# Kernel optimization log

Measured on AMD Instinct MI355X. Metric: run time of the kernel, lower is better.

## Reference

```python
import jax, jax.numpy as jnp
import numpy as np

THRESH = 0.5
DECAY = 0.2
D_IN = 784
H1 = 2048
H2 = 10
K = 10
U = D_IN + H1
L = 128
B = 1024


def setup_inputs() -> dict:
    key = jax.random.key(0)
    ks = jax.random.split(key, 6)
    inp = jax.random.uniform(ks[0], (B, D_IN), dtype=jnp.float32)
    W1 = jax.random.normal(ks[1], (H1, D_IN), dtype=jnp.float32) * 0.05
    b1 = jnp.zeros((H1,), dtype=jnp.float32)
    W2 = jax.random.normal(ks[2], (H2, H1), dtype=jnp.float32) * 0.05
    b2 = jnp.zeros((H2,), dtype=jnp.float32)
    # core_mem_all[k][u][0] -> sparse-ish per-unit vector, [1] -> count
    core_mem_vec = (jax.random.uniform(ks[3], (K, U, L)) > 0.7).astype(jnp.float32)
    core_mem_cnt = jax.random.randint(ks[4], (K, U), 0, 5).astype(jnp.int32)
    return {"input": inp, "W1": W1, "b1": b1, "W2": W2, "b2": b2,
            "core_mem_vec": core_mem_vec, "core_mem_cnt": core_mem_cnt,
            "time_window": 20}


def act_fun(mem):
    # spike = Heaviside(mem - thresh)
    return (mem > THRESH).astype(mem.dtype)


def reference(input, W1, b1, W2, b2, core_mem_vec, core_mem_cnt, time_window):
    batch, d_in = input.shape
    h1 = W1.shape[0]
    h2 = W2.shape[0]
    Lv = core_mem_vec.shape[-1]

    # Precompute, per (core k, unit u): contribution to count_add_1 / count_add_2
    # when unit u spikes. count_add_1 += (last nonzero index of temp) - 1 when cnt>0;
    # count_add_2 += cnt when cnt>0. Sum over cores up front (loop order irrelevant).
    nz = core_mem_vec != 0                                     # [K,U,L]
    has = nz.any(-1)
    last_idx = Lv - 1 - jnp.argmax(nz[..., ::-1].astype(jnp.int32), axis=-1)  # [K,U]
    active = (core_mem_cnt > 0) & has
    val1 = jnp.where(active, last_idx - 1, 0).sum(0).astype(jnp.float32)      # [U]
    val2 = jnp.where(core_mem_cnt > 0, core_mem_cnt, 0).sum(0).astype(jnp.float32)
    v1x, v1h = val1[:d_in], val1[d_in:]
    v2x, v2h = val2[:d_in], val2[d_in:]

    key = jax.random.key(42)

    def step(carry, t):
        h1m, h1s, h2m, h2s, h2sum, a1, a2, cs = carry
        # Bernoulli rate encoding of the input image
        x = (input > jax.random.uniform(jax.random.fold_in(key, t), input.shape)).astype(jnp.float32)
        # mem_update: mem = mem*decay*(1-spike) + W x + b ; spike = mem > thresh
        h1m = h1m * DECAY * (1.0 - h1s) + x @ W1.T + b1
        h1s = act_fun(h1m)
        h2m = h2m * DECAY * (1.0 - h2s) + h1s @ W2.T + b2
        h2s = act_fun(h2m)
        h2sum = h2sum + h2s
        # vectorized core-memory gather/count: sum per-unit precomputed values
        # over all spiking units, across the batch
        xs = x.sum(0)      # [784] spike counts per input unit this step
        hs = h1s.sum(0)    # [h1]
        a1 = a1 + xs @ v1x + hs @ v1h
        a2 = a2 + xs @ v2x + hs @ v2h
        cs = cs + xs.sum() + hs.sum()
        return (h1m, h1s, h2m, h2s, h2sum, a1, a2, cs), None

    z1 = jnp.zeros((batch, h1), dtype=jnp.float32)
    z2 = jnp.zeros((batch, h2), dtype=jnp.float32)
    carry = (z1, z1, z2, z2, z2, jnp.float32(0), jnp.float32(0), jnp.float32(0))
    carry, _ = jax.lax.scan(step, carry, jnp.arange(time_window))
    _, _, _, _, h2sum, a1, a2, cs = carry
    outputs = h2sum / time_window
    return outputs, a1, a2, cs
```

## Files before the change

### kernel.cpp

```cpp
#include <hip/hip_runtime.h>
#include <cstdint>
#include <cstddef>

static constexpr int D_IN = 784;
static constexpr int H1   = 2048;
static constexpr int H2   = 10;
static constexpr int KK   = 10;
static constexpr int UU   = 2832;
static constexpr int LL   = 128;
static constexpr int BB   = 1024;
static constexpr int TT   = 20;
static constexpr int HALF = BB * D_IN / 2;
static constexpr int NCH  = 25;
static constexpr int NLIMB = 3;
static constexpr int XA_T  = 32 * NCH * 64;
static constexpr int BITS_T = BB * 64;
static constexpr int PANEL = NCH * NLIMB * 64;
static constexpr int NPART_GEN = 2000;
static constexpr int NPART_H1  = 256;
static constexpr int NPART = NPART_GEN + NPART_H1;

static constexpr int BLK_VALS  = UU / 4;
static constexpr int BLK_W2T   = H1 / 256;
static constexpr int BLK_LIMBS = (64 * NCH * 64) / 256;
static constexpr int BLK_TRANS = 16 * 13;
static constexpr int SETUP_BLOCKS = BLK_VALS + BLK_W2T + BLK_LIMBS + BLK_TRANS;

typedef int v4i  __attribute__((ext_vector_type(4)));
typedef int v16i __attribute__((ext_vector_type(16)));

#define MFMA_I8 __builtin_amdgcn_mfma_i32_32x32x32_i8

__device__ __forceinline__ uint32_t rotl32(uint32_t x, int d) {
  return (x << d) | (x >> (32 - d));
}
__device__ __forceinline__ void threefry2x32(uint32_t k0, uint32_t k1,
                                             uint32_t& x0, uint32_t& x1) {
  uint32_t ks2 = k0 ^ k1 ^ 0x1BD11BDAu;
  x0 += k0; x1 += k1;
#define TF_R(r) { x0 += x1; x1 = rotl32(x1, (r)); x1 ^= x0; }
  TF_R(13) TF_R(15) TF_R(26) TF_R(6)
  x0 += k1;  x1 += ks2 + 1u;
  TF_R(17) TF_R(29) TF_R(16) TF_R(24)
  x0 += ks2; x1 += k0 + 2u;
  TF_R(13) TF_R(15) TF_R(26) TF_R(6)
  x0 += k0;  x1 += k1 + 3u;
  TF_R(17) TF_R(29) TF_R(16) TF_R(24)
  x0 += k1;  x1 += ks2 + 4u;
  TF_R(13) TF_R(15) TF_R(26) TF_R(6)
  x0 += ks2; x1 += k0 + 5u;
#undef TF_R
}
__device__ __forceinline__ float bits_to_unif(uint32_t b) {
  uint32_t fb = (b >> 9) | 0x3F800000u;
  return __uint_as_float(fb) - 1.0f;
}

__device__ __forceinline__ double wave_red(double v) {
  #pragma unroll
  for (int off = 32; off > 0; off >>= 1) v += __shfl_down(v, off, 64);
  return v;
}
__device__ __forceinline__ void block_store3(double s0, double s1, double s2,
                                             double* slot) {
  __shared__ double lds[3][8];
  int lane = threadIdx.x & 63, w = threadIdx.x >> 6;
  int nw = (int)(blockDim.x >> 6);
  s0 = wave_red(s0); s1 = wave_red(s1); s2 = wave_red(s2);
  if (lane == 0) { lds[0][w] = s0; lds[1][w] = s1; lds[2][w] = s2; }
  __syncthreads();
  if (threadIdx.x == 0) {
    double t0 = 0, t1 = 0, t2 = 0;
    for (int i = 0; i < nw; i++) { t0 += lds[0][i]; t1 += lds[1][i]; t2 += lds[2][i]; }
    slot[0] = t0; slot[1] = t1; slot[2] = t2;
  }
}

__global__ __launch_bounds__(256)
void setup(const float* __restrict__ cmv, const int* __restrict__ cmc,
           float* __restrict__ v1, float* __restrict__ v2,
           const float* __restrict__ W2, float* __restrict__ W2T,
           const float* __restrict__ W1, v4i* __restrict__ W1L,
           const float* __restrict__ input, float2* __restrict__ inT2) {
  int bx = blockIdx.x;
  if (bx < BLK_VALS) {
    int u = bx * 4 + (threadIdx.x >> 6);
    int lane = threadIdx.x & 63;
    float acc1 = 0.0f, acc2 = 0.0f;
    for (int k = 0; k < KK; k++) {
      const float* p = cmv + ((size_t)k * UU + u) * LL;
      float a = p[lane];
      float b = p[lane + 64];
      unsigned long long mlo = __ballot(a != 0.0f);
      unsigned long long mhi = __ballot(b != 0.0f);
      int c = cmc[k * UU + u];
      if (c > 0) {
        int last = mhi ? (127 - __builtin_clzll(mhi))
                       : (mlo ? (63 - __builtin_clzll(mlo)) : -1);
        if (last >= 0) acc1 += (float)(last - 1);
        acc2 += (float)c;
      }
    }
    if (lane == 0) { v1[u] = acc1; v2[u] = acc2; }
  } else if (bx < BLK_VALS + BLK_W2T) {
    int i = (bx - BLK_VALS) * 256 + threadIdx.x;
    #pragma unroll
    for (int j = 0; j < H2; j++) W2T[i * H2 + j] = W2[j * H1 + i];
  } else if (bx < BLK_VALS + BLK_W2T + BLK_LIMBS) {
    int tid = (bx - BLK_VALS - BLK_W2T) * 256 + threadIdx.x;
    int lane = tid & 63;
    int tc = tid >> 6;
    int n = ((tc / NCH) << 5) + (lane & 31);
    int chunk = tc % NCH;
    int k0 = chunk * 32 + (lane >> 5) * 16;
    union { v4i v; signed char b[16]; } d[NLIMB];
    #pragma unroll
    for (int j = 0; j < 16; j++) {
      long long F = 0;
      int k = k0 + j;
      if (k < D_IN) {
        double w = (double)W1[(size_t)n * D_IN + k];
        F = llround(w * 0x1p24);
        if (F >  8355711LL) F =  8355711LL;
        if (F < -8421504LL) F = -8421504LL;
      }
      #pragma unroll
      for (int l = 0; l < NLIMB; l++) {
        int dig = (int)((F + 128) & 255) - 128;
        d[l].b[j] = (signed char)dig;
        F = (F - dig) >> 8;
      }
    }
    #pragma unroll
    for (int l = 0; l < NLIMB; l++) W1L[(size_t)(tc * NLIMB + l) * 64 + lane] = d[l].v;
  } else {
    int tile = bx - (BLK_VALS + BLK_W2T + BLK_LIMBS);
    int tm = tile / 13, tk = tile % 13;
    int mb = tm * 32, k0 = tk * 64;
    int ncol = (tk == 12) ? 16 : 64;
    __shared__ float ts[64][65];
    int tid = threadIdx.x;
    if (tk == 12) {
      for (int idx = tid; idx < 64 * 4; idx += 256) {
        int r = idx >> 2, c4 = idx & 3;
        int m = mb + (r & 31) + ((r >> 5) << 9);
        const float4* src = (const float4*)(input + (size_t)m * D_IN + k0 + c4 * 4);
        float4 vq = *src;
        ts[r][c4 * 4 + 0] = vq.x; ts[r][c4 * 4 + 1] = vq.y;
        ts[r][c4 * 4 + 2] = vq.z; ts[r][c4 * 4 + 3] = vq.w;
      }
    } else {
      for (int idx = tid; idx < 64 * 16; idx += 256) {
        int r = idx >> 4, c4 = idx & 15;
        int m = mb + (r & 31) + ((r >> 5) << 9);
        const float4* src = (const float4*)(input + (size_t)m * D_IN + k0 + c4 * 4);
        float4 vq = *src;
        ts[r][c4 * 4 + 0] = vq.x; ts[r][c4 * 4 + 1] = vq.y;
        ts[r][c4 * 4 + 2] = vq.z; ts[r][c4 * 4 + 3] = vq.w;
      }
    }
    __syncthreads();
    for (int idx = tid; idx < ncol * 32; idx += 256) {
      int kr = idx >> 5, mc = idx & 31;
      inT2[(size_t)(k0 + kr) * 512 + mb + mc] =
          make_float2(ts[mc][kr], ts[32 + mc][kr]);
    }
  }
}

__global__ __launch_bounds__(256)
void gen_all(const float2* __restrict__ inT2, v4i* __restrict__ XA,
             const float* __restrict__ v1, const float* __restrict__ v2,
             double* __restrict__ gpart) {
  int t  = blockIdx.x / 100;
  int gw = (blockIdx.x % 100) * 4 + (threadIdx.x >> 6);
  int lane = threadIdx.x & 63;
  int mtile = gw / NCH, chunk = gw - mtile * NCH;
  int m = (mtile << 5) + (lane & 31);
  int k0 = chunk * 32 + (lane >> 5) * 16;
  uint32_t f0 = 0u, f1 = (uint32_t)t;
  threefry2x32(0u, 42u, f0, f1);
  union { v4i v; unsigned char b[16]; } r0, r1;
  double s0 = 0, s1 = 0, s2 = 0;
  v4i* XA_t = XA + (size_t)t * XA_T;
  if (k0 < D_IN) {
    #pragma unroll
    for (int j = 0; j < 16; j++) {
      int k = k0 + j;
      uint32_t c0 = (uint32_t)(m * D_IN + k), c1 = c0 + (uint32_t)HALF;
      threefry2x32(f0, f1, c0, c1);
      float u0 = bits_to_unif(c0), u1 = bits_to_unif(c1);
      float2 iv = inT2[(size_t)k * 512 + m];
      unsigned char x0 = (iv.x > u0) ? 1 : 0;
      unsigned char x1 = (iv.y > u1) ? 1 : 0;
      r0.b[j] = x0; r1.b[j] = x1;
      double xsum = (double)(x0 + x1);
      s0 += xsum * (double)v1[k];
      s1 += xsum * (double)v2[k];
      s2 += xsum;
    }
  } else {
    r0.v = (v4i){0, 0, 0, 0};
    r1.v = (v4i){0, 0, 0, 0};
  }
  XA_t[(size_t)(mtile * NCH + chunk) * 64 + lane] = r0.v;
  XA_t[(size_t)((mtile + 16) * NCH + chunk) * 64 + lane] = r1.v;
  block_store3(s0, s1, s2, gpart + 3 * (size_t)blockIdx.x);
}

__global__ __launch_bounds__(512, 2)
void h1_all(const v4i* __restrict__ XA, const v4i* __restrict__ W1L,
            const float* __restrict__ b1, uint32_t* __restrict__ bits,
            const float* __restrict__ v1, const float* __restrict__ v2,
            double* __restrict__ gpart) {
  extern __shared__ v4i bl[];
  int lane = threadIdx.x & 63, wv = threadIdx.x >> 6;
  int id = blockIdx.x + (blockIdx.y << 6);
  int xcd = id & 7;
  int idx = id >> 3;
  int ntile = (idx << 1) | (xcd >> 2);
  int mtg = xcd & 3;
  int mt = mtg * 8 + wv;
  {
    const v4i* wp = W1L + (size_t)ntile * PANEL;
    for (int i = threadIdx.x; i < PANEL; i += 512) bl[i] = wp[i];
  }
  __syncthreads();

  int col = lane & 31;
  int gn = (ntile << 5) + col;
  float bias = b1[gn];
  double v1n = (double)v1[D_IN + gn], v2n = (double)v2[D_IN + gn];
  int scnt = 0;
  float mreg[16];
  #pragma unroll
  for (int r = 0; r < 16; r++) mreg[r] = 0.0f;

  const v4i* bq = bl + lane;
  const v4i* a0 = XA + (size_t)mt * (NCH * 64) + lane;
  const v4i* a1 = a0 + XA_T;
  v4i Ab[3][2], Bb[2][3];
  Ab[0][0] = a0[0];   Ab[0][1] = a1[0];
  Ab[1][0] = a0[64];  Ab[1][1] = a1[64];
  Ab[2][0] = a0[128]; Ab[2][1] = a1[128];
  Bb[0][0] = bq[0];   Bb[0][1] = bq[64];  Bb[0][2] = bq[128];
  Bb[1][0] = bq[192]; Bb[1][1] = bq[256]; Bb[1][2] = bq[320];

  if (wv & 1) __builtin_amdgcn_s_sleep(96);

  #pragma unroll 1
  for (int tp = 0; tp < TT / 2; tp++) {
    const v4i* a0n = (tp < TT / 2 - 1) ? (a0 + 2 * XA_T)
                                       : (XA + (size_t)mt * (NCH * 64) + lane);
    const v4i* a1n = a0n + XA_T;
    v16i c00 = {}, c01 = {}, c02 = {};
    v16i c10 = {}, c11 = {}, c12 = {};
    __builtin_amdgcn_s_setprio(1);
    #pragma unroll
    for (int c = 0; c < NCH; c++) {
      v4i A0 = Ab[c % 3][0], A1 = Ab[c % 3][1];
      v4i B0 = Bb[c % 2][0], B1 = Bb[c % 2][1], B2 = Bb[c % 2][2];
      c00 = MFMA_I8(A0, B0, c00, 0, 0, 0);
      c10 = MFMA_I8(A1, B0, c10, 0, 0, 0);
      c01 = MFMA_I8(A0, B1, c01, 0, 0, 0);
      c11 = MFMA_I8(A1, B1, c11, 0, 0, 0);
      c02 = MFMA_I8(A0, B2, c02, 0, 0, 0);
      c12 = MFMA_I8(A1, B2, c12, 0, 0, 0);
      if (c <= 21) {
        Ab[c % 3][0] = a0[(c + 3) * 64];
        Ab[c % 3][1] = a1[(c + 3) * 64];
      } else {
        const int nc = (c == 24) ? 0 : (c - 21);
        Ab[c % 3][0] = a0n[nc * 64];
        Ab[c % 3][1] = a1n[nc * 64];
      }
      {
        const int bc = (c <= 22) ? (c + 2) : ((c == 23) ? 1 : 0);
        const v4i* br = bq + (size_t)bc * (NLIMB * 64);
        Bb[c % 2][0] = br[0]; Bb[c % 2][1] = br[64]; Bb[c % 2][2] = br[128];
      }
    }
    __builtin_amdgcn_s_setprio(0);
    a0 = a0n; a1 = a1n;
    #pragma unroll
    for (int half = 0; half < 2; half++) {
      const v16i& q0 = half ? c10 : c00;
      const v16i& q1 = half ? c11 : c01;
      const v16i& q2 = half ? c12 : c02;
      uint32_t* btm = bits + (size_t)(2 * tp + half) * BITS_T
                    + ((size_t)mt << 5) * 64 + ntile;
      #pragma unroll
      for (int r = 0; r < 16; r++) {
        int val = (int)((uint32_t)q0[r] + ((uint32_t)q1[r] << 8)
                        + ((uint32_t)q2[r] << 16));
        float dot = (float)val * 0x1p-24f + bias;
        float mp = mreg[r];
        float mnew = (mp > 0.5f) ? dot : fmaf(mp, 0.2f, dot);
        bool s = (mnew > 0.5f);
        mreg[r] = mnew;
        unsigned long long bm = __ballot(s);
        int rowA = (r & 3) + 8 * (r >> 2);
        if ((lane & 31) == 0)
          btm[(size_t)(rowA + ((lane >> 5) << 2)) * 64] = (uint32_t)(bm >> (lane & 32));
        scnt += s ? 1 : 0;
      }
    }
  }
  double sc = (double)scnt;
  block_store3(sc * v1n, sc * v2n, sc, gpart + 3 * (size_t)(NPART_GEN + id));
}

__global__ __launch_bounds__(256)
void h2_all(const uint32_t* __restrict__ bits, const float* __restrict__ W2T,
            const float* __restrict__ b2, const double* __restrict__ gpart,
            float* __restrict__ out) {
  int lane = threadIdx.x & 63, wq = threadIdx.x >> 6;
  int b0 = blockIdx.x * 2;
  float w[8][10];
  #pragma unroll
  for (int c = 0; c < 8; c++) {
    int n = (wq << 9) + (c << 6) + lane;
    #pragma unroll
    for (int j = 0; j < 10; j++) w[c][j] = W2T[(size_t)n * H2 + j];
  }
  float m = 0.0f, sp = 0.0f, sm = 0.0f;
  float b2v = (lane < 10) ? b2[lane] : 0.0f;
  __shared__ float part[4][2][10];
  #pragma unroll 1
  for (int t = 0; t < TT; t++) {
    const uint32_t* bt = bits + (size_t)t * BITS_T;
    #pragma unroll
    for (int r = 0; r < 2; r++) {
      uint32_t myw = bt[(size_t)(b0 + r) * 64 + (wq << 4) + (lane & 15)];
      float p[10];
      #pragma unroll
      for (int j = 0; j < 10; j++) p[j] = 0.0f;
      #pragma unroll
      for (int c = 0; c < 8; c++) {
        uint32_t wd = __shfl(myw, (c << 1) + (lane >> 5), 64);
        float f = (float)((wd >> (lane & 31)) & 1u);
        #pragma unroll
        for (int j = 0; j < 10; j++) p[j] += f * w[c][j];
      }
      #pragma unroll
      for (int j = 0; j < 10; j++) {
        float v = p[j];
        #pragma unroll
        for (int off = 32; off > 0; off >>= 1) v += __shfl_xor(v, off, 64);
        p[j] = v;
      }
      if (lane == 0) {
        #pragma unroll
        for (int j = 0; j < 10; j++) part[wq][r][j] = p[j];
      }
    }
    __syncthreads();
    if (wq < 2 && lane < 10) {
      float red = part[0][wq][lane] + part[1][wq][lane]
                + part[2][wq][lane] + part[3][wq][lane];
      m = m * 0.2f * (1.0f - sp) + red + b2v;
      sp = (m > 0.5f) ? 1.0f : 0.0f;
      sm += sp;
    }
    __syncthreads();
  }
  if (wq < 2 && lane < 10)
    out[(size_t)(b0 + wq) * H2 + lane] = (float)((double)sm / (double)TT);

  if (blockIdx.x == 0) {
    double t0 = 0, t1 = 0, t2 = 0;
    for (int i = threadIdx.x; i < NPART; i += 256) {
      t0 += gpart[3 * (size_t)i];
      t1 += gpart[3 * (size_t)i + 1];
      t2 += gpart[3 * (size_t)i + 2];
    }
    __shared__ double fin[3][4];
    t0 = wave_red(t0); t1 = wave_red(t1); t2 = wave_red(t2);
    if (lane == 0) { fin[0][wq] = t0; fin[1][wq] = t1; fin[2][wq] = t2; }
    __syncthreads();
    if (threadIdx.x == 0) {
      double a = 0, b = 0, cc = 0;
      #pragma unroll
      for (int i = 0; i < 4; i++) { a += fin[0][i]; b += fin[1][i]; cc += fin[2][i]; }
      out[(size_t)BB * H2 + 0] = (float)a;
      out[(size_t)BB * H2 + 1] = (float)b;
      out[(size_t)BB * H2 + 2] = (float)cc;
    }
  }
}

extern "C" void kernel_launch(void* const* d_in, const int* in_sizes, int n_in,
                              void* d_out, int out_size, void* d_ws, size_t ws_size,
                              hipStream_t stream) {
  (void)in_sizes; (void)n_in; (void)out_size; (void)ws_size;
  const float* input = (const float*)d_in[0];
  const float* W1    = (const float*)d_in[1];
  const float* b1    = (const float*)d_in[2];
  const float* W2    = (const float*)d_in[3];
  const float* b2    = (const float*)d_in[4];
  const float* cmv   = (const float*)d_in[5];
  const int*   cmc   = (const int*)d_in[6];

  char* base = (char*)d_ws;
  float*  v1   = (float*)(base + 0);
  float*  v2   = (float*)(base + 11328);
  float*  W2T  = (float*)(base + 22656);
  v4i*    W1L  = (v4i*)(base + 104576);
  v4i*    XA   = (v4i*)(base + 5019776);
  uint32_t* bits = (uint32_t*)(base + 21403776);
  float2* inT2 = (float2*)(base + 26646656);
  double* gpart = (double*)(base + 29857920);

  setup<<<SETUP_BLOCKS, 256, 0, stream>>>(cmv, cmc, v1, v2, W2, W2T, W1, W1L,
                                          input, inT2);
  gen_all<<<TT * 100, 256, 0, stream>>>(inT2, XA, v1, v2, gpart);
  h1_all<<<dim3(64, 4), 512, PANEL * 16, stream>>>(XA, W1L, b1, bits, v1, v2,
                                                   gpart);
  h2_all<<<BB / 2, 256, 0, stream>>>(bits, W2T, b2, gpart, (float*)d_out);
}
```

Measured before the change: 288.3 us.

## Switch h1 GEMM to 16x16x64 int8 MFMA tiles with smaller panels

Rebuilds the first-layer integer GEMM around 16x16x64 i8 MFMA instead of 32x32x32, re-laying out the W1 limb panels and the spike-input XA buffer into 16-row tiles with 64-wide K steps. The h1 kernel now runs twice as many blocks with smaller LDS panels and higher occupancy (launch bounds 4 per CU), loops over all timesteps without manual register prefetch, and writes 16-bit spike masks. The inT2 scratch area is aliased with the bits buffer to shrink the workspace. This trades the explicit software pipelining for more concurrent waves and smaller accumulators, with the risk of more memory latency exposure per MFMA.

```diff
diff --git a/kernel.cpp b/kernel.cpp
--- a/kernel.cpp
+++ b/kernel.cpp
@@ -11,25 +11,25 @@
 static constexpr int BB   = 1024;
 static constexpr int TT   = 20;
 static constexpr int HALF = BB * D_IN / 2;
-static constexpr int NCH  = 25;
+static constexpr int KS   = 13;
 static constexpr int NLIMB = 3;
-static constexpr int XA_T  = 32 * NCH * 64;
-static constexpr int BITS_T = BB * 64;
-static constexpr int PANEL = NCH * NLIMB * 64;
-static constexpr int NPART_GEN = 2000;
-static constexpr int NPART_H1  = 256;
+static constexpr int NT16 = 128;
+static constexpr int MT16 = 64;
+static constexpr int PANEL16 = KS * NLIMB * 64;
+static constexpr int XA_MT = KS * 64;
+static constexpr int NPART_GEN = 2080;
+static constexpr int NPART_H1  = 512;
 static constexpr int NPART = NPART_GEN + NPART_H1;
 
 static constexpr int BLK_VALS  = UU / 4;
 static constexpr int BLK_W2T   = H1 / 256;
-static constexpr int BLK_LIMBS = (64 * NCH * 64) / 256;
+static constexpr int BLK_LIMBS = (NT16 * KS) / 4;
 static constexpr int BLK_TRANS = 16 * 13;
 static constexpr int SETUP_BLOCKS = BLK_VALS + BLK_W2T + BLK_LIMBS + BLK_TRANS;
 
 typedef int v4i  __attribute__((ext_vector_type(4)));
-typedef int v16i __attribute__((ext_vector_type(16)));
-
-#define MFMA_I8 __builtin_amdgcn_mfma_i32_32x32x32_i8
+
+#define MFMA16 __builtin_amdgcn_mfma_i32_16x16x64_i8
 
 __device__ __forceinline__ uint32_t rotl32(uint32_t x, int d) {
   return (x << d) | (x >> (32 - d));
@@ -109,17 +109,17 @@
   } else if (bx < BLK_VALS + BLK_W2T + BLK_LIMBS) {
     int tid = (bx - BLK_VALS - BLK_W2T) * 256 + threadIdx.x;
     int lane = tid & 63;
-    int tc = tid >> 6;
-    int n = ((tc / NCH) << 5) + (lane & 31);
-    int chunk = tc % NCH;
-    int k0 = chunk * 32 + (lane >> 5) * 16;
+    int tw = tid >> 6;
+    int nt = tw / KS, s = tw - nt * KS;
+    int n = (nt << 4) + (lane & 15);
+    int k0 = (s << 6) + ((lane >> 4) << 4);
+    bool valid = (k0 < D_IN);
     union { v4i v; signed char b[16]; } d[NLIMB];
     #pragma unroll
     for (int j = 0; j < 16; j++) {
       long long F = 0;
-      int k = k0 + j;
-      if (k < D_IN) {
-        double w = (double)W1[(size_t)n * D_IN + k];
+      if (valid) {
+        double w = (double)W1[(size_t)n * D_IN + k0 + j];
         F = llround(w * 0x1p24);
         if (F >  8355711LL) F =  8355711LL;
         if (F < -8421504LL) F = -8421504LL;
@@ -132,7 +132,8 @@
       }
     }
     #pragma unroll
-    for (int l = 0; l < NLIMB; l++) W1L[(size_t)(tc * NLIMB + l) * 64 + lane] = d[l].v;
+    for (int l = 0; l < NLIMB; l++)
+      W1L[(size_t)((nt * KS + s) * NLIMB + l) * 64 + lane] = d[l].v;
   } else {
     int tile = bx - (BLK_VALS + BLK_W2T + BLK_LIMBS);
     int tm = tile / 13, tk = tile % 13;
@@ -140,24 +141,14 @@
     int ncol = (tk == 12) ? 16 : 64;
     __shared__ float ts[64][65];
     int tid = threadIdx.x;
-    if (tk == 12) {
-      for (int idx = tid; idx < 64 * 4; idx += 256) {
-        int r = idx >> 2, c4 = idx & 3;
-        int m = mb + (r & 31) + ((r >> 5) << 9);
-        const float4* src = (const float4*)(input + (size_t)m * D_IN + k0 + c4 * 4);
-        float4 vq = *src;
-        ts[r][c4 * 4 + 0] = vq.x; ts[r][c4 * 4 + 1] = vq.y;
-        ts[r][c4 * 4 + 2] = vq.z; ts[r][c4 * 4 + 3] = vq.w;
-      }
-    } else {
-      for (int idx = tid; idx < 64 * 16; idx += 256) {
-        int r = idx >> 4, c4 = idx & 15;
-        int m = mb + (r & 31) + ((r >> 5) << 9);
-        const float4* src = (const float4*)(input + (size_t)m * D_IN + k0 + c4 * 4);
-        float4 vq = *src;
-        ts[r][c4 * 4 + 0] = vq.x; ts[r][c4 * 4 + 1] = vq.y;
-        ts[r][c4 * 4 + 2] = vq.z; ts[r][c4 * 4 + 3] = vq.w;
-      }
+    int nc4 = (tk == 12) ? 4 : 16;
+    for (int idx = tid; idx < 64 * nc4; idx += 256) {
+      int r = idx / nc4, c4 = idx % nc4;
+      int m = mb + (r & 31) + ((r >> 5) << 9);
+      const float4* src = (const float4*)(input + (size_t)m * D_IN + k0 + c4 * 4);
+      float4 vq = *src;
+      ts[r][c4 * 4 + 0] = vq.x; ts[r][c4 * 4 + 1] = vq.y;
+      ts[r][c4 * 4 + 2] = vq.z; ts[r][c4 * 4 + 3] = vq.w;
     }
     __syncthreads();
     for (int idx = tid; idx < ncol * 32; idx += 256) {
@@ -172,17 +163,17 @@
 void gen_all(const float2* __restrict__ inT2, v4i* __restrict__ XA,
              const float* __restrict__ v1, const float* __restrict__ v2,
              double* __restrict__ gpart) {
-  int t  = blockIdx.x / 100;
-  int gw = (blockIdx.x % 100) * 4 + (threadIdx.x >> 6);
+  int gw = blockIdx.x * 4 + (threadIdx.x >> 6);
   int lane = threadIdx.x & 63;
-  int mtile = gw / NCH, chunk = gw - mtile * NCH;
-  int m = (mtile << 5) + (lane & 31);
-  int k0 = chunk * 32 + (lane >> 5) * 16;
+  int t = gw / (32 * KS);
+  int rem = gw - t * (32 * KS);
+  int mt = rem / KS, s = rem - mt * KS;
+  int m = (mt << 4) + (lane & 15);
+  int k0 = (s << 6) + ((lane >> 4) << 4);
   uint32_t f0 = 0u, f1 = (uint32_t)t;
   threefry2x32(0u, 42u, f0, f1);
   union { v4i v; unsigned char b[16]; } r0, r1;
   double s0 = 0, s1 = 0, s2 = 0;
-  v4i* XA_t = XA + (size_t)t * XA_T;
   if (k0 < D_IN) {
     #pragma unroll
     for (int j = 0; j < 16; j++) {
@@ -203,106 +194,84 @@
     r0.v = (v4i){0, 0, 0, 0};
     r1.v = (v4i){0, 0, 0, 0};
   }
-  XA_t[(size_t)(mtile * NCH + chunk) * 64 + lane] = r0.v;
-  XA_t[(size_t)((mtile + 16) * NCH + chunk) * 64 + lane] = r1.v;
+  XA[(size_t)((t * MT16 + mt) * KS + s) * 64 + lane] = r0.v;
+  XA[(size_t)((t * MT16 + mt + 32) * KS + s) * 64 + lane] = r1.v;
   block_store3(s0, s1, s2, gpart + 3 * (size_t)blockIdx.x);
 }
 
-__global__ __launch_bounds__(512, 2)
+__global__ __launch_bounds__(512, 4)
 void h1_all(const v4i* __restrict__ XA, const v4i* __restrict__ W1L,
-            const float* __restrict__ b1, uint32_t* __restrict__ bits,
+            const float* __restrict__ b1, uint16_t* __restrict__ bits16,
             const float* __restrict__ v1, const float* __restrict__ v2,
             double* __restrict__ gpart) {
   extern __shared__ v4i bl[];
   int lane = threadIdx.x & 63, wv = threadIdx.x >> 6;
   int id = blockIdx.x + (blockIdx.y << 6);
   int xcd = id & 7;
-  int idx = id >> 3;
-  int ntile = (idx << 1) | (xcd >> 2);
-  int mtg = xcd & 3;
-  int mt = mtg * 8 + wv;
+  int ntb = ((id >> 3) << 1) | (xcd >> 2);
+  int mg = xcd & 3;
+  int mt0 = (mg << 4) + (wv << 1);
   {
-    const v4i* wp = W1L + (size_t)ntile * PANEL;
-    for (int i = threadIdx.x; i < PANEL; i += 512) bl[i] = wp[i];
+    const v4i* wp = W1L + (size_t)ntb * PANEL16;
+    for (int i = threadIdx.x; i < PANEL16; i += 512) bl[i] = wp[i];
   }
   __syncthreads();
 
-  int col = lane & 31;
-  int gn = (ntile << 5) + col;
+  int col = lane & 15;
+  int gn = (ntb << 4) + col;
   float bias = b1[gn];
   double v1n = (double)v1[D_IN + gn], v2n = (double)v2[D_IN + gn];
   int scnt = 0;
-  float mreg[16];
-  #pragma unroll
-  for (int r = 0; r < 16; r++) mreg[r] = 0.0f;
-
+  float m00 = 0, m01 = 0, m02 = 0, m03 = 0;
+  float m10 = 0, m11 = 0, m12 = 0, m13 = 0;
   const v4i* bq = bl + lane;
-  const v4i* a0 = XA + (size_t)mt * (NCH * 64) + lane;
-  const v4i* a1 = a0 + XA_T;
-  v4i Ab[3][2], Bb[2][3];
-  Ab[0][0] = a0[0];   Ab[0][1] = a1[0];
-  Ab[1][0] = a0[64];  Ab[1][1] = a1[64];
-  Ab[2][0] = a0[128]; Ab[2][1] = a1[128];
-  Bb[0][0] = bq[0];   Bb[0][1] = bq[64];  Bb[0][2] = bq[128];
-  Bb[1][0] = bq[192]; Bb[1][1] = bq[256]; Bb[1][2] = bq[320];
-
-  if (wv & 1) __builtin_amdgcn_s_sleep(96);
+  int rowg = (lane >> 4) << 2;
 
   #pragma unroll 1
-  for (int tp = 0; tp < TT / 2; tp++) {
-    const v4i* a0n = (tp < TT / 2 - 1) ? (a0 + 2 * XA_T)
-                                       : (XA + (size_t)mt * (NCH * 64) + lane);
-    const v4i* a1n = a0n + XA_T;
-    v16i c00 = {}, c01 = {}, c02 = {};
-    v16i c10 = {}, c11 = {}, c12 = {};
+  for (int t = 0; t < TT; t++) {
+    const v4i* a0 = XA + (size_t)((t * MT16 + mt0) * KS) * 64 + lane;
+    const v4i* a1 = a0 + KS * 64;
+    v4i c00 = {}, c01 = {}, c02 = {};
+    v4i c10 = {}, c11 = {}, c12 = {};
     __builtin_amdgcn_s_setprio(1);
     #pragma unroll
-    for (int c = 0; c < NCH; c++) {
-      v4i A0 = Ab[c % 3][0], A1 = Ab[c % 3][1];
-      v4i B0 = Bb[c % 2][0], B1 = Bb[c % 2][1], B2 = Bb[c % 2][2];
-      c00 = MFMA_I8(A0, B0, c00, 0, 0, 0);
-      c10 = MFMA_I8(A1, B0, c10, 0, 0, 0);
-      c01 = MFMA_I8(A0, B1, c01, 0, 0, 0);
-      c11 = MFMA_I8(A1, B1, c11, 0, 0, 0);
-      c02 = MFMA_I8(A0, B2, c02, 0, 0, 0);
-      c12 = MFMA_I8(A1, B2, c12, 0, 0, 0);
-      if (c <= 21) {
-        Ab[c % 3][0] = a0[(c + 3) * 64];
-        Ab[c % 3][1] = a1[(c + 3) * 64];
-      } else {
-        const int nc = (c == 24) ? 0 : (c - 21);
-        Ab[c % 3][0] = a0n[nc * 64];
-        Ab[c % 3][1] = a1n[nc * 64];
-      }
-      {
-        const int bc = (c <= 22) ? (c + 2) : ((c == 23) ? 1 : 0);
-        const v4i* br = bq + (size_t)bc * (NLIMB * 64);
-        Bb[c % 2][0] = br[0]; Bb[c % 2][1] = br[64]; Bb[c % 2][2] = br[128];
-      }
+    for (int s = 0; s < KS; s++) {
+      v4i A0 = a0[s * 64], A1 = a1[s * 64];
+      v4i B0 = bq[(s * NLIMB + 0) * 64];
+      v4i B1 = bq[(s * NLIMB + 1) * 64];
+      v4i B2 = bq[(s * NLIMB + 2) * 64];
+      c00 = MFMA16(A0, B0, c00, 0, 0, 0);
+      c10 = MFMA16(A1, B0, c10, 0, 0, 0);
+      c01 = MFMA16(A0, B1, c01, 0, 0, 0);
+      c11 = MFMA16(A1, B1, c11, 0, 0, 0);
+      c02 = MFMA16(A0, B2, c02, 0, 0, 0);
+      c12 = MFMA16(A1, B2, c12, 0, 0, 0);
     }
     __builtin_amdgcn_s_setprio(0);
-    a0 = a0n; a1 = a1n;
-    #pragma unroll
-    for (int half = 0; half < 2; half++) {
-      const v16i& q0 = half ? c10 : c00;
-      const v16i& q1 = half ? c11 : c01;
-      const v16i& q2 = half ? c12 : c02;
-      uint32_t* btm = bits + (size_t)(2 * tp + half) * BITS_T
-                    + ((size_t)mt << 5) * 64 + ntile;
-      #pragma unroll
-      for (int r = 0; r < 16; r++) {
+    #pragma unroll
+    for (int tile = 0; tile < 2; tile++) {
+      const v4i& q0 = tile ? c10 : c00;
+      const v4i& q1 = tile ? c11 : c01;
+      const v4i& q2 = tile ? c12 : c02;
+      int gmb = ((mt0 + tile) << 4);
+      uint16_t* bp = bits16 + ((size_t)t * BB + gmb) * NT16 + ntb;
+      #pragma unroll
+      for (int r = 0; r < 4; r++) {
         int val = (int)((uint32_t)q0[r] + ((uint32_t)q1[r] << 8)
                         + ((uint32_t)q2[r] << 16));
         float dot = (float)val * 0x1p-24f + bias;
-        float mp = mreg[r];
+        float mp = tile ? (r == 0 ? m10 : r == 1 ? m11 : r == 2 ? m12 : m13)
+                        : (r == 0 ? m00 : r == 1 ? m01 : r == 2 ? m02 : m03);
         float mnew = (mp > 0.5f) ? dot : fmaf(mp, 0.2f, dot);
-        bool s = (mnew > 0.5f);
-        mreg[r] = mnew;
-        unsigned long long bm = __ballot(s);
-        int rowA = (r & 3) + 8 * (r >> 2);
-        if ((lane & 31) == 0)
-          btm[(size_t)(rowA + ((lane >> 5) << 2)) * 64] = (uint32_t)(bm >> (lane & 32));
-        scnt += s ? 1 : 0;
+        bool sp = (mnew > 0.5f);
+        if (tile) { if (r == 0) m10 = mnew; else if (r == 1) m11 = mnew;
+                    else if (r == 2) m12 = mnew; else m13 = mnew; }
+        else      { if (r == 0) m00 = mnew; else if (r == 1) m01 = mnew;
+                    else if (r == 2) m02 = mnew; else m03 = mnew; }
+        unsigned long long bm = __ballot(sp);
+        if ((lane & 15) == 0)
+          bp[(size_t)(rowg + r) * NT16] = (uint16_t)(bm >> lane);
+        scnt += sp ? 1 : 0;
       }
     }
   }
@@ -328,7 +297,7 @@
   __shared__ float part[4][2][10];
   #pragma unroll 1
   for (int t = 0; t < TT; t++) {
-    const uint32_t* bt = bits + (size_t)t * BITS_T;
+    const uint32_t* bt = bits + (size_t)t * (BB * 64);
     #pragma unroll
     for (int r = 0; r < 2; r++) {
       uint32_t myw = bt[(size_t)(b0 + r) * 64 + (wq << 4) + (lane & 15)];
@@ -406,15 +375,17 @@
   float*  v2   = (float*)(base + 11328);
   float*  W2T  = (float*)(base + 22656);
   v4i*    W1L  = (v4i*)(base + 104576);
-  v4i*    XA   = (v4i*)(base + 5019776);
-  uint32_t* bits = (uint32_t*)(base + 21403776);
-  float2* inT2 = (float2*)(base + 26646656);
-  double* gpart = (double*)(base + 29857920);
+  v4i*    XA   = (v4i*)(base + 5216384);
+  char*   bitsb = base + 22255744;
+  double* gpart = (double*)(base + 27498624);
+  float2* inT2 = (float2*)bitsb;
+  uint16_t* bits16 = (uint16_t*)bitsb;
+  uint32_t* bits32 = (uint32_t*)bitsb;
 
   setup<<<SETUP_BLOCKS, 256, 0, stream>>>(cmv, cmc, v1, v2, W2, W2T, W1, W1L,
                                           input, inT2);
-  gen_all<<<TT * 100, 256, 0, stream>>>(inT2, XA, v1, v2, gpart);
-  h1_all<<<dim3(64, 4), 512, PANEL * 16, stream>>>(XA, W1L, b1, bits, v1, v2,
-                                                   gpart);
-  h2_all<<<BB / 2, 256, 0, stream>>>(bits, W2T, b2, gpart, (float*)d_out);
-}
+  gen_all<<<NPART_GEN, 256, 0, stream>>>(inT2, XA, v1, v2, gpart);
+  h1_all<<<dim3(64, 8), 512, PANEL16 * 16, stream>>>(XA, W1L, b1, bits16, v1, v2,
+                                                     gpart);
+  h2_all<<<BB / 2, 256, 0, stream>>>(bits32, W2T, b2, gpart, (float*)d_out);
+}
```

Result: no change. 283.8 us (-1.6%).
